# Kernel optimization log

Hardware: AMD Instinct MI355X
Metric: run time of the kernel (lower is better)

Reference implementation:

```python
import jax, jax.numpy as jnp
import numpy as np

B = 8          # graphs per batch
N_PER = 8192   # nodes per graph (equal-sized graphs -> static topk shapes)
N = B * N_PER  # 65536 total nodes
DEG = 16
E = DEG * N    # 1,048,576 edges
C = 64         # conv_width


def setup_inputs() -> dict:
    key = jax.random.key(0)
    ks = jax.random.split(key, 32)
    epg = E // B
    g = jnp.arange(E, dtype=jnp.int32) // epg            # graph id per edge
    src = jax.random.randint(ks[0], (E,), 0, N_PER, dtype=jnp.int32) + g * N_PER
    dst = jax.random.randint(ks[1], (E,), 0, N_PER, dtype=jnp.int32) + g * N_PER

    def w(k, shape, fan_in):
        return (jax.random.normal(k, shape) / np.sqrt(fan_in)).astype(jnp.float32)

    inp = {
        "x": jax.random.normal(ks[2], (N, 2), dtype=jnp.float32),
        "edge_index": jnp.stack([src, dst]),
        # SAGEConv i: out = mean_agg @ wl + x @ wr + b
        "w1l": w(ks[3], (2, C), 2),  "w1r": w(ks[4], (2, C), 2),  "b1": jnp.zeros((C,), jnp.float32),
        "w2l": w(ks[5], (C, C), C),  "w2r": w(ks[6], (C, C), C),  "b2": jnp.zeros((C,), jnp.float32),
        "w3l": w(ks[7], (C, C), C),  "w3r": w(ks[8], (C, C), C),  "b3": jnp.zeros((C,), jnp.float32),
        # GCNConv
        "w4": w(ks[9], (C, C), C),   "b4": jnp.zeros((C,), jnp.float32),
        # TopKPooling score vectors
        "p1": w(ks[10], (C,), C), "p2": w(ks[11], (C,), C),
        "p3": w(ks[12], (C,), C), "p4": w(ks[13], (C,), C),
        # MLP head
        "lw1": w(ks[14], (2 * C, 128), 2 * C), "lb1": jnp.zeros((128,), jnp.float32),
        "lw2": w(ks[15], (128, 64), 128),      "lb2": jnp.zeros((64,), jnp.float32),
        "lw3": w(ks[16], (64, 1), 64),         "lb3": jnp.zeros((1,), jnp.float32),
    }
    return inp


def _sage(x, src, dst, em, wl, wr, b):
    # PyG SAGEConv: lin_l(mean of in-neighbors) + lin_r(x); masked edges contribute 0
    n = x.shape[0]
    s = jax.ops.segment_sum(x[src] * em[:, None], dst, num_segments=n)
    cnt = jax.ops.segment_sum(em, dst, num_segments=n)
    mean = s / jnp.maximum(cnt, 1.0)[:, None]
    return mean @ wl + x @ wr + b


def _gcn(x, src, dst, em, w, b):
    # PyG GCNConv with added self-loops, symmetric normalization
    n = x.shape[0]
    xw = x @ w
    deg = jax.ops.segment_sum(em, dst, num_segments=n) + 1.0  # +1 self-loop
    dinv = jax.lax.rsqrt(deg)
    coef = (dinv[src] * dinv[dst] * em)[:, None]
    agg = jax.ops.segment_sum(xw[src] * coef, dst, num_segments=n)
    return agg + xw / deg[:, None] + b  # self-loop term: deg^-0.5 * deg^-0.5


def _pool(x, src, dst, em, p, nb):
    # TopKPooling(ratio=0.5): score = x.p/||p||, keep top half per graph, scale by tanh
    n = x.shape[0]
    npg = n // nb
    k = npg // 2
    score = x @ p / jnp.linalg.norm(p)
    _, idx = jax.lax.top_k(score.reshape(nb, npg), k)          # [nb, k] local idx
    perm = (idx + (jnp.arange(nb, dtype=idx.dtype) * npg)[:, None]).reshape(-1)
    xn = x[perm] * jnp.tanh(score[perm])[:, None]
    o2n = jnp.full((n,), -1, jnp.int32).at[perm].set(jnp.arange(nb * k, dtype=jnp.int32))
    ns, nd = o2n[src], o2n[dst]
    nm = em * ((ns >= 0) & (nd >= 0)).astype(em.dtype)         # filter_adj via mask
    return xn, jnp.maximum(ns, 0), jnp.maximum(nd, 0), nm


def _readout(x, nb):
    # cat([global_max_pool, global_mean_pool])
    npg = x.shape[0] // nb
    batch = jnp.repeat(jnp.arange(nb), npg)
    mx = jax.ops.segment_max(x, batch, num_segments=nb)
    mn = jax.ops.segment_sum(x, batch, num_segments=nb) / npg
    return jnp.concatenate([mx, mn], axis=1)


def reference(x, edge_index, w1l, w1r, b1, w2l, w2r, b2, w3l, w3r, b3, w4, b4,
              p1, p2, p3, p4, lw1, lb1, lw2, lb2, lw3, lb3):
    src, dst = edge_index[0], edge_index[1]
    em = jnp.ones((src.shape[0],), jnp.float32)

    h = jax.nn.relu(_sage(x, src, dst, em, w1l, w1r, b1))
    h, src, dst, em = _pool(h, src, dst, em, p1, B)
    x1 = _readout(h, B)

    h = jax.nn.relu(_sage(h, src, dst, em, w2l, w2r, b2))
    h, src, dst, em = _pool(h, src, dst, em, p2, B)
    x2 = _readout(h, B)

    h = jax.nn.relu(_sage(h, src, dst, em, w3l, w3r, b3))
    h, src, dst, em = _pool(h, src, dst, em, p3, B)
    x3 = _readout(h, B)  # computed but unused, matching original (x = x1 + x2)

    h = jax.nn.relu(_gcn(h, src, dst, em, w4, b4))
    h, src, dst, em = _pool(h, src, dst, em, p4, B)
    x4 = _readout(h, B)  # computed but unused, matching original

    z = x1 + x2
    z = jax.nn.relu(z @ lw1 + lb1)
    z = jax.nn.relu(z @ lw2 + lb2)
    return z @ lw3 + lb3  # [B, 1]
```

## Files before the change

### kernel.cpp

```cpp
#include <hip/hip_runtime.h>
#include <stdint.h>
#include <math.h>

#define NB 8
#define NPG0 8192
#define EPG 131072
#define P1 16
#define MAXDEG 64

__global__ __launch_bounds__(1024)
void k_aggp(const int* __restrict__ src, const int* __restrict__ dst,
            const float* __restrict__ x, float* __restrict__ partial)
{
    __shared__ float acc[3 * 2048];
    int b = blockIdx.x;
    int g = b >> 6, qq = (b >> 4) & 3, sl = b & 15;
    int tid = threadIdx.x;
    float4* acc4 = (float4*)acc;
    float4 z4 = make_float4(0.f, 0.f, 0.f, 0.f);
    acc4[tid] = z4;
    if (tid < 512) acc4[1024 + tid] = z4;
    __syncthreads();
    int e0 = g * EPG + sl * (EPG / P1);
    int nbase = g * NPG0 + qq * 2048;
    #pragma unroll
    for (int k = 0; k < EPG / P1 / 1024; ++k) {
        int e = e0 + k * 1024 + tid;
        int d = dst[e];
        unsigned local = (unsigned)(d - nbase);
        if (local < 2048u) {
            int s = src[e];
            float2 xv = reinterpret_cast<const float2*>(x)[s];
            atomicAdd(&acc[local], xv.x);
            atomicAdd(&acc[2048 + local], xv.y);
            atomicAdd(&acc[4096 + local], 1.0f);
        }
    }
    __syncthreads();
    float4* o = (float4*)(partial + (size_t)b * 6144);
    o[tid] = acc4[tid];
    if (tid < 512) o[1024 + tid] = acc4[1024 + tid];
}

__global__ void k_aggr(const float* __restrict__ partial, float* __restrict__ agg,
                       int n0)
{
    int t = blockIdx.x * 256 + threadIdx.x;
    if (t >= 3 * n0) return;
    int c = t / n0, node = t - c * n0;
    int g = node >> 13, local = node & (NPG0 - 1);
    int qq = local >> 11, ll = local & 2047;
    const float* p = partial + (size_t)(g * 64 + qq * 16) * 6144 + c * 2048 + ll;
    float s = 0.0f;
    #pragma unroll
    for (int q = 0; q < P1; ++q) s += p[(size_t)q * 6144];
    agg[t] = s;
}

__global__ void k_sage1(const float* __restrict__ x, const float* __restrict__ agg,
                        const float* __restrict__ w1l, const float* __restrict__ w1r,
                        const float* __restrict__ b1, const float* __restrict__ p1,
                        float* __restrict__ h1, float* __restrict__ s1, int n)
{
    int tid  = threadIdx.x;
    int lane = tid & 63;
    int i    = blockIdx.x * 4 + (tid >> 6);
    if (i >= n) return;
    float c   = agg[2 * n + i];
    float inv = 1.0f / fmaxf(c, 1.0f);
    float m0 = agg[i] * inv, m1 = agg[n + i] * inv;
    float2 xv = reinterpret_cast<const float2*>(x)[i];
    float h = m0 * w1l[lane] + m1 * w1l[64 + lane]
            + xv.x * w1r[lane] + xv.y * w1r[64 + lane] + b1[lane];
    h = fmaxf(h, 0.0f);
    h1[i * 64 + lane] = h;
    float pv = p1[lane];
    float num = h * pv, nrm = pv * pv;
    #pragma unroll
    for (int o = 32; o; o >>= 1) {
        num += __shfl_xor(num, o);
        nrm += __shfl_xor(nrm, o);
    }
    if (lane == 0) s1[i] = num / sqrtf(nrm);
}

__device__ __forceinline__ unsigned scan1024(unsigned val, volatile unsigned* ws)
{
    int tid = threadIdx.x, lane = tid & 63, wid = tid >> 6;
    unsigned sc = val;
    #pragma unroll
    for (int off = 1; off < 64; off <<= 1) {
        unsigned t = __shfl_up(sc, off);
        if (lane >= off) sc += t;
    }
    if (lane == 63) ws[wid] = sc;
    __syncthreads();
    if (tid < 16) {
        unsigned w = ws[tid];
        #pragma unroll
        for (int off = 1; off < 16; off <<= 1) {
            unsigned t = __shfl_up(w, off);
            if (tid >= off) w += t;
        }
        ws[tid] = w;
    }
    __syncthreads();
    return sc + (wid ? ws[wid - 1] : 0u);
}

template <int NPG>
__global__ __launch_bounds__(1024)
void k_pool_sel(const float* __restrict__ score, int* __restrict__ n2o,
                int* __restrict__ o2n, int K)
{
    __shared__ unsigned key[NPG];
    __shared__ unsigned hist[1024];
    __shared__ unsigned ws[16];
    __shared__ unsigned long long cand[1024];
    __shared__ int sT1, sR1, sT2, sR2, selCnt, c3;
    int g = blockIdx.x, tid = threadIdx.x;
    if (tid == 0) { selCnt = 0; c3 = 0; }
    hist[tid] = 0u;
    if (o2n) for (int i = tid; i < NPG; i += 1024) o2n[g * NPG + i] = -1;
    __syncthreads();
    for (int i = tid; i < NPG; i += 1024) {
        unsigned b = __float_as_uint(score[g * NPG + i]);
        unsigned u = (b & 0x80000000u) ? ~b : (b | 0x80000000u);
        key[i] = u;
        atomicAdd(&hist[u >> 22], 1u);
    }
    __syncthreads();
    {
        unsigned S = scan1024(hist[1023 - tid], ws);
        int b = 1023 - tid;
        unsigned h = hist[b];
        if (S >= (unsigned)K && S - h < (unsigned)K) { sT1 = b; sR1 = K - (int)(S - h); }
    }
    __syncthreads();
    int T1 = sT1, R1 = sR1;
    for (int i = tid; i < NPG; i += 1024) {
        if ((int)(key[i] >> 22) > T1) {
            int s = atomicAdd(&selCnt, 1);
            int oldid = g * NPG + i;
            n2o[g * K + s] = oldid;
            if (o2n) o2n[oldid] = g * K + s;
        }
    }
    __syncthreads();
    hist[tid] = 0u;
    __syncthreads();
    for (int i = tid; i < NPG; i += 1024)
        if ((int)(key[i] >> 22) == T1) atomicAdd(&hist[(key[i] >> 12) & 1023u], 1u);
    __syncthreads();
    {
        unsigned S = scan1024(hist[1023 - tid], ws);
        int b = 1023 - tid;
        unsigned h = hist[b];
        if (S >= (unsigned)R1 && S - h < (unsigned)R1) { sT2 = b; sR2 = R1 - (int)(S - h); }
    }
    __syncthreads();
    int T2 = sT2, R2 = sR2;
    for (int i = tid; i < NPG; i += 1024) {
        unsigned u = key[i];
        if ((int)(u >> 22) == T1) {
            int b2 = (int)((u >> 12) & 1023u);
            if (b2 > T2) {
                int s = atomicAdd(&selCnt, 1);
                int oldid = g * NPG + i;
                n2o[g * K + s] = oldid;
                if (o2n) o2n[oldid] = g * K + s;
            } else if (b2 == T2) {
                int c = atomicAdd(&c3, 1);
                if (c < 1024)
                    cand[c] = ((unsigned long long)u << 32) | (unsigned)(NPG - 1 - i);
            }
        }
    }
    __syncthreads();
    int M = min(c3, 1024);
    for (int t = tid; t < M; t += 1024) {
        unsigned long long k0 = cand[t];
        int rank = 0;
        for (int j = 0; j < M; ++j) rank += (cand[j] > k0);
        if (rank < R2) {
            int i = NPG - 1 - (int)(k0 & 0xFFFFFFFFu);
            int s = atomicAdd(&selCnt, 1);
            int oldid = g * NPG + i;
            n2o[g * K + s] = oldid;
            if (o2n) o2n[oldid] = g * K + s;
        }
    }
}

__global__ void k_gather(const float* __restrict__ h, const int* __restrict__ n2o,
                         const float* __restrict__ sc, float* __restrict__ hp, int n)
{
    int idx = blockIdx.x * 256 + threadIdx.x;
    int j = idx >> 4, cg = idx & 15;
    if (j >= n) return;
    int oldid = n2o[j];
    float t = tanhf(sc[oldid]);
    float4 v = reinterpret_cast<const float4*>(h)[oldid * 16 + cg];
    v.x *= t; v.y *= t; v.z *= t; v.w *= t;
    reinterpret_cast<float4*>(hp)[idx] = v;
}

__global__ __launch_bounds__(1024)
void k_readout_p(const float* __restrict__ h, const int* __restrict__ n2o,
                 const float* __restrict__ sc, int npg,
                 float* __restrict__ pmx, float* __restrict__ psm)
{
    int g = blockIdx.x >> 4, sl = blockIdx.x & 15;
    int tid = threadIdx.x;
    int cg = tid & 15, rsl = tid >> 4;
    int rpb = npg >> 4;
    float4 mx = make_float4(-INFINITY, -INFINITY, -INFINITY, -INFINITY);
    float4 sm = make_float4(0.f, 0.f, 0.f, 0.f);
    for (int r = rsl; r < rpb; r += 64) {
        int row = g * npg + sl * rpb + r;
        int oldid = n2o ? n2o[row] : row;
        float4 v = reinterpret_cast<const float4*>(h)[oldid * 16 + cg];
        if (sc) {
            float t = tanhf(sc[oldid]);
            v.x *= t; v.y *= t; v.z *= t; v.w *= t;
        }
        mx.x = fmaxf(mx.x, v.x); mx.y = fmaxf(mx.y, v.y);
        mx.z = fmaxf(mx.z, v.z); mx.w = fmaxf(mx.w, v.w);
        sm.x += v.x; sm.y += v.y; sm.z += v.z; sm.w += v.w;
    }
    __shared__ float4 smx[1024], ssm[1024];
    smx[tid] = mx; ssm[tid] = sm;
    __syncthreads();
    for (int s = 32; s >= 1; s >>= 1) {
        if (rsl < s) {
            float4 a = smx[tid], b = smx[tid + s * 16];
            a.x = fmaxf(a.x, b.x); a.y = fmaxf(a.y, b.y);
            a.z = fmaxf(a.z, b.z); a.w = fmaxf(a.w, b.w);
            smx[tid] = a;
            float4 c = ssm[tid], d = ssm[tid + s * 16];
            c.x += d.x; c.y += d.y; c.z += d.z; c.w += d.w;
            ssm[tid] = c;
        }
        __syncthreads();
    }
    if (rsl == 0) {
        reinterpret_cast<float4*>(pmx)[(g * 16 + sl) * 16 + cg] = smx[tid];
        reinterpret_cast<float4*>(psm)[(g * 16 + sl) * 16 + cg] = ssm[tid];
    }
}

__global__ void k_build(const int* __restrict__ src, const int* __restrict__ dst,
                        const int* __restrict__ o2n, int* __restrict__ cnt,
                        int* __restrict__ slots, int E)
{
    int e = blockIdx.x * 256 + threadIdx.x;
    if (e >= E) return;
    int ns = o2n[src[e]], nd = o2n[dst[e]];
    if (ns >= 0 && nd >= 0) {
        int pos = atomicAdd(&cnt[nd], 1);
        if (pos < MAXDEG) slots[nd * MAXDEG + pos] = ns;
    }
}

__global__ __launch_bounds__(256)
void k_sage2(const float* __restrict__ hp, const int* __restrict__ cnt,
             const int* __restrict__ slots,
             const float* __restrict__ w2l, const float* __restrict__ w2r,
             const float* __restrict__ b2, const float* __restrict__ p2,
             float* __restrict__ h2, float* __restrict__ s2)
{
    __shared__ float Xs[64 * 128];
    __shared__ float Wt[64 * 128];
    int tid = threadIdx.x, blk = blockIdx.x;

    #pragma unroll
    for (int i = 0; i < 32; ++i) {
        int idx = i * 256 + tid;
        int k = idx >> 6, c = idx & 63;
        float w = (k < 64) ? w2l[k * 64 + c] : w2r[(k - 64) * 64 + c];
        int slot = (k >> 2) ^ ((c >> 2) & 7);
        Wt[c * 128 + slot * 4 + (k & 3)] = w;
    }

    {
        int n = tid >> 2, p = tid & 3;
        int j = blk * 64 + n;
        int dg = cnt[j];
        int lim = min(dg, MAXDEG);
        const int* sl = slots + j * MAXDEG;
        const float4* hp4 = reinterpret_cast<const float4*>(hp);
        float4 a[4];
        #pragma unroll
        for (int u = 0; u < 4; ++u) a[u] = make_float4(0.f, 0.f, 0.f, 0.f);
        int e = 0;
        for (; e + 1 < lim; e += 2) {
            int r0 = sl[e] * 16 + p * 4;
            int r1 = sl[e + 1] * 16 + p * 4;
            float4 v[4], u4[4];
            #pragma unroll
            for (int u = 0; u < 4; ++u) v[u] = hp4[r0 + u];
            #pragma unroll
            for (int u = 0; u < 4; ++u) u4[u] = hp4[r1 + u];
            #pragma unroll
            for (int u = 0; u < 4; ++u) {
                a[u].x += v[u].x + u4[u].x; a[u].y += v[u].y + u4[u].y;
                a[u].z += v[u].z + u4[u].z; a[u].w += v[u].w + u4[u].w;
            }
        }
        if (e < lim) {
            int r0 = sl[e] * 16 + p * 4;
            #pragma unroll
            for (int u = 0; u < 4; ++u) {
                float4 v = hp4[r0 + u];
                a[u].x += v.x; a[u].y += v.y; a[u].z += v.z; a[u].w += v.w;
            }
        }
        float inv = 1.0f / fmaxf((float)dg, 1.0f);
        int swz = (n >> 2) & 7;
        float4* X4 = reinterpret_cast<float4*>(Xs);
        #pragma unroll
        for (int u = 0; u < 4; ++u) {
            float4 m = a[u];
            m.x *= inv; m.y *= inv; m.z *= inv; m.w *= inv;
            X4[n * 32 + ((p * 4 + u) ^ swz)] = m;
        }
        #pragma unroll
        for (int u = 0; u < 4; ++u)
            X4[n * 32 + ((16 + p * 4 + u) ^ swz)] = hp4[j * 16 + p * 4 + u];
    }
    __syncthreads();

    int rt = tid >> 4, ct = tid & 15;
    int r0 = rt * 4, c0 = ct * 4;
    int swa = rt & 7, swb = ct & 7;
    const float4* Xf = reinterpret_cast<const float4*>(Xs);
    const float4* Wf = reinterpret_cast<const float4*>(Wt);
    float acc[4][4];
    #pragma unroll
    for (int i = 0; i < 4; ++i)
        #pragma unroll
        for (int jq = 0; jq < 4; ++jq) acc[i][jq] = 0.f;
    #pragma unroll 8
    for (int ks = 0; ks < 32; ++ks) {
        float4 aa[4], bb[4];
        #pragma unroll
        for (int i = 0; i < 4; ++i) aa[i] = Xf[(r0 + i) * 32 + (ks ^ swa)];
        #pragma unroll
        for (int jq = 0; jq < 4; ++jq) bb[jq] = Wf[(c0 + jq) * 32 + (ks ^ swb)];
        #pragma unroll
        for (int i = 0; i < 4; ++i)
            #pragma unroll
            for (int jq = 0; jq < 4; ++jq)
                acc[i][jq] += aa[i].x * bb[jq].x + aa[i].y * bb[jq].y
                            + aa[i].z * bb[jq].z + aa[i].w * bb[jq].w;
    }

    float4 b2v = reinterpret_cast<const float4*>(b2)[ct];
    float4 p2v = reinterpret_cast<const float4*>(p2)[ct];
    float nrm = p2v.x * p2v.x + p2v.y * p2v.y + p2v.z * p2v.z + p2v.w * p2v.w;
    float sp[4];
    float4* h2f = reinterpret_cast<float4*>(h2);
    #pragma unroll
    for (int i = 0; i < 4; ++i) {
        float4 o;
        o.x = fmaxf(acc[i][0] + b2v.x, 0.f);
        o.y = fmaxf(acc[i][1] + b2v.y, 0.f);
        o.z = fmaxf(acc[i][2] + b2v.z, 0.f);
        o.w = fmaxf(acc[i][3] + b2v.w, 0.f);
        h2f[(blk * 64 + r0 + i) * 16 + ct] = o;
        sp[i] = o.x * p2v.x + o.y * p2v.y + o.z * p2v.z + o.w * p2v.w;
    }
    #pragma unroll
    for (int o = 1; o < 16; o <<= 1) {
        #pragma unroll
        for (int i = 0; i < 4; ++i) sp[i] += __shfl_xor(sp[i], o);
        nrm += __shfl_xor(nrm, o);
    }
    if (ct == 0) {
        float r = rsqrtf(nrm);
        #pragma unroll
        for (int i = 0; i < 4; ++i) s2[blk * 64 + r0 + i] = sp[i] * r;
    }
}

__global__ __launch_bounds__(128)
void k_mlp(const float* __restrict__ pmx1, const float* __restrict__ psm1,
           const float* __restrict__ pmx2, const float* __restrict__ psm2,
           int npg1, int npg2,
           const float* __restrict__ lw1, const float* __restrict__ lb1,
           const float* __restrict__ lw2, const float* __restrict__ lb2,
           const float* __restrict__ lw3, const float* __restrict__ lb3,
           float* __restrict__ out)
{
    __shared__ float z[NB][128], o1[NB][128], o2[NB][64];
    int tid = threadIdx.x;
    for (int g = 0; g < NB; ++g) {
        float v;
        if (tid < 64) {
            float m1 = -INFINITY, m2 = -INFINITY;
            #pragma unroll
            for (int sl = 0; sl < 16; ++sl) {
                m1 = fmaxf(m1, pmx1[(g * 16 + sl) * 64 + tid]);
                m2 = fmaxf(m2, pmx2[(g * 16 + sl) * 64 + tid]);
            }
            v = m1 + m2;
        } else {
            int ch = tid - 64;
            float s1 = 0.f, s2 = 0.f;
            #pragma unroll
            for (int sl = 0; sl < 16; ++sl) {
                s1 += psm1[(g * 16 + sl) * 64 + ch];
                s2 += psm2[(g * 16 + sl) * 64 + ch];
            }
            v = s1 / (float)npg1 + s2 / (float)npg2;
        }
        z[g][tid] = v;
    }
    __syncthreads();
    for (int g = 0; g < NB; ++g) {
        float a = lb1[tid];
        for (int i = 0; i < 128; ++i) a += z[g][i] * lw1[i * 128 + tid];
        o1[g][tid] = fmaxf(a, 0.0f);
    }
    __syncthreads();
    if (tid < 64) {
        for (int g = 0; g < NB; ++g) {
            float a = lb2[tid];
            for (int i = 0; i < 128; ++i) a += o1[g][i] * lw2[i * 64 + tid];
            o2[g][tid] = fmaxf(a, 0.0f);
        }
    }
    __syncthreads();
    if (tid < NB) {
        int g = tid;
        float a = lb3[0];
        for (int i = 0; i < 64; ++i) a += o2[g][i] * lw3[i];
        out[g] = a;
    }
}

extern "C" void kernel_launch(void* const* d_in, const int* in_sizes, int n_in,
                              void* d_out, int out_size, void* d_ws, size_t ws_size,
                              hipStream_t stream)
{
    (void)n_in; (void)out_size; (void)ws_size;
    const float* x   = (const float*)d_in[0];
    const int*   ei  = (const int*)d_in[1];
    const float* w1l = (const float*)d_in[2];
    const float* w1r = (const float*)d_in[3];
    const float* b1  = (const float*)d_in[4];
    const float* w2l = (const float*)d_in[5];
    const float* w2r = (const float*)d_in[6];
    const float* b2  = (const float*)d_in[7];
    const float* p1  = (const float*)d_in[13];
    const float* p2  = (const float*)d_in[14];
    const float* lw1 = (const float*)d_in[17];
    const float* lb1 = (const float*)d_in[18];
    const float* lw2 = (const float*)d_in[19];
    const float* lb2 = (const float*)d_in[20];
    const float* lw3 = (const float*)d_in[21];
    const float* lb3 = (const float*)d_in[22];

    const int N0   = in_sizes[0] / 2;
    const int E    = in_sizes[1] / 2;
    const int K1   = NPG0 / 2;
    const int N1   = NB * K1;
    const int K2   = K1 / 2;

    const int* src = ei;
    const int* dst = ei + E;

    char* w = (char*)d_ws;
    auto alloc = [&](size_t bytes) -> char* {
        char* p = w;
        w += (bytes + 255) & ~(size_t)255;
        return p;
    };
    float* partial = (float*)alloc((size_t)NB * 4 * P1 * 6144 * 4);
    float* agg   = (float*)alloc((size_t)3 * N0 * 4);
    int*   cnt2  = (int*)alloc((size_t)N1 * 4);
    int*   slots = (int*)alloc((size_t)N1 * MAXDEG * 4);
    float* h1    = (float*)alloc((size_t)N0 * 64 * 4);
    float* s1    = (float*)alloc((size_t)N0 * 4);
    int*   o2n1  = (int*)alloc((size_t)N0 * 4);
    int*   n2o1  = (int*)alloc((size_t)N1 * 4);
    float* h1p   = (float*)alloc((size_t)N1 * 64 * 4);
    float* h2    = (float*)alloc((size_t)N1 * 64 * 4);
    float* s2    = (float*)alloc((size_t)N1 * 4);
    int*   n2o2  = (int*)alloc((size_t)(NB * K2) * 4);
    float* pmx1  = (float*)alloc((size_t)NB * 16 * 64 * 4);
    float* psm1  = (float*)alloc((size_t)NB * 16 * 64 * 4);
    float* pmx2  = (float*)alloc((size_t)NB * 16 * 64 * 4);
    float* psm2  = (float*)alloc((size_t)NB * 16 * 64 * 4);

    hipMemsetAsync(cnt2, 0, (size_t)N1 * 4, stream);

    k_aggp<<<NB * 4 * P1, 1024, 0, stream>>>(src, dst, x, partial);
    k_aggr<<<(3 * N0 + 255) / 256, 256, 0, stream>>>(partial, agg, N0);
    k_sage1<<<N0 / 4, 256, 0, stream>>>(x, agg, w1l, w1r, b1, p1, h1, s1, N0);
    k_pool_sel<8192><<<NB, 1024, 0, stream>>>(s1, n2o1, o2n1, K1);
    k_gather<<<N1 * 16 / 256, 256, 0, stream>>>(h1, n2o1, s1, h1p, N1);
    k_readout_p<<<NB * 16, 1024, 0, stream>>>(h1p, nullptr, nullptr, K1, pmx1, psm1);
    k_build<<<E / 256, 256, 0, stream>>>(src, dst, o2n1, cnt2, slots, E);
    k_sage2<<<N1 / 64, 256, 0, stream>>>(h1p, cnt2, slots, w2l, w2r, b2, p2, h2, s2);
    k_pool_sel<4096><<<NB, 1024, 0, stream>>>(s2, n2o2, nullptr, K2);
    k_readout_p<<<NB * 16, 1024, 0, stream>>>(h2, n2o2, s2, K2, pmx2, psm2);
    k_mlp<<<1, 128, 0, stream>>>(pmx1, psm1, pmx2, psm2, K1, K2,
                                 lw1, lb1, lw2, lb2, lw3, lb3, (float*)d_out);
}
```

Measured before the change: 144.8 us.

## Fuse partial reduction into SAGE1 scoring and recompute h1 in pooled readout

Merges the partial-sum reduction with the first SAGE layer's score computation so the full h1 tensor is never written. Only per-node mean features (float2) are stored, and the pooled h1p is recomputed from them inside a fused gather+readout kernel. This removes roughly 16MB of h1 traffic and two kernel launches. The edge loops in aggregation and adjacency build are also vectorized to int4 loads, which adds some per-thread serial work and recomputes the 64-wide dot product twice.

```diff
diff --git a/kernel.cpp b/kernel.cpp
--- a/kernel.cpp
+++ b/kernel.cpp
@@ -23,17 +23,24 @@
     __syncthreads();
     int e0 = g * EPG + sl * (EPG / P1);
     int nbase = g * NPG0 + qq * 2048;
-    #pragma unroll
-    for (int k = 0; k < EPG / P1 / 1024; ++k) {
-        int e = e0 + k * 1024 + tid;
-        int d = dst[e];
-        unsigned local = (unsigned)(d - nbase);
-        if (local < 2048u) {
-            int s = src[e];
-            float2 xv = reinterpret_cast<const float2*>(x)[s];
-            atomicAdd(&acc[local], xv.x);
-            atomicAdd(&acc[2048 + local], xv.y);
-            atomicAdd(&acc[4096 + local], 1.0f);
+    const float2* x2 = reinterpret_cast<const float2*>(x);
+    #pragma unroll
+    for (int k = 0; k < 2; ++k) {
+        int e = e0 + (k * 1024 + tid) * 4;
+        int4 d4 = *reinterpret_cast<const int4*>(dst + e);
+        unsigned l0 = (unsigned)(d4.x - nbase), l1 = (unsigned)(d4.y - nbase);
+        unsigned l2 = (unsigned)(d4.z - nbase), l3 = (unsigned)(d4.w - nbase);
+        bool v0 = l0 < 2048u, v1 = l1 < 2048u, v2 = l2 < 2048u, v3 = l3 < 2048u;
+        if (v0 | v1 | v2 | v3) {
+            int4 s4 = *reinterpret_cast<const int4*>(src + e);
+            if (v0) { float2 xv = x2[s4.x]; atomicAdd(&acc[l0], xv.x);
+                      atomicAdd(&acc[2048 + l0], xv.y); atomicAdd(&acc[4096 + l0], 1.0f); }
+            if (v1) { float2 xv = x2[s4.y]; atomicAdd(&acc[l1], xv.x);
+                      atomicAdd(&acc[2048 + l1], xv.y); atomicAdd(&acc[4096 + l1], 1.0f); }
+            if (v2) { float2 xv = x2[s4.z]; atomicAdd(&acc[l2], xv.x);
+                      atomicAdd(&acc[2048 + l2], xv.y); atomicAdd(&acc[4096 + l2], 1.0f); }
+            if (v3) { float2 xv = x2[s4.w]; atomicAdd(&acc[l3], xv.x);
+                      atomicAdd(&acc[2048 + l3], xv.y); atomicAdd(&acc[4096 + l3], 1.0f); }
         }
     }
     __syncthreads();
@@ -42,46 +49,36 @@
     if (tid < 512) o[1024 + tid] = acc4[1024 + tid];
 }
 
-__global__ void k_aggr(const float* __restrict__ partial, float* __restrict__ agg,
-                       int n0)
-{
-    int t = blockIdx.x * 256 + threadIdx.x;
-    if (t >= 3 * n0) return;
-    int c = t / n0, node = t - c * n0;
+__global__ __launch_bounds__(256)
+void k_sage1f(const float* __restrict__ partial, const float* __restrict__ x,
+              const float* __restrict__ w1l, const float* __restrict__ w1r,
+              const float* __restrict__ b1, const float* __restrict__ p1,
+              float2* __restrict__ mv, float* __restrict__ s1)
+{
+    int tid = threadIdx.x;
+    int node = blockIdx.x * 256 + tid;
     int g = node >> 13, local = node & (NPG0 - 1);
     int qq = local >> 11, ll = local & 2047;
-    const float* p = partial + (size_t)(g * 64 + qq * 16) * 6144 + c * 2048 + ll;
-    float s = 0.0f;
-    #pragma unroll
-    for (int q = 0; q < P1; ++q) s += p[(size_t)q * 6144];
-    agg[t] = s;
-}
-
-__global__ void k_sage1(const float* __restrict__ x, const float* __restrict__ agg,
-                        const float* __restrict__ w1l, const float* __restrict__ w1r,
-                        const float* __restrict__ b1, const float* __restrict__ p1,
-                        float* __restrict__ h1, float* __restrict__ s1, int n)
-{
-    int tid  = threadIdx.x;
-    int lane = tid & 63;
-    int i    = blockIdx.x * 4 + (tid >> 6);
-    if (i >= n) return;
-    float c   = agg[2 * n + i];
-    float inv = 1.0f / fmaxf(c, 1.0f);
-    float m0 = agg[i] * inv, m1 = agg[n + i] * inv;
-    float2 xv = reinterpret_cast<const float2*>(x)[i];
-    float h = m0 * w1l[lane] + m1 * w1l[64 + lane]
-            + xv.x * w1r[lane] + xv.y * w1r[64 + lane] + b1[lane];
-    h = fmaxf(h, 0.0f);
-    h1[i * 64 + lane] = h;
-    float pv = p1[lane];
-    float num = h * pv, nrm = pv * pv;
-    #pragma unroll
-    for (int o = 32; o; o >>= 1) {
-        num += __shfl_xor(num, o);
-        nrm += __shfl_xor(nrm, o);
-    }
-    if (lane == 0) s1[i] = num / sqrtf(nrm);
+    const float* p = partial + (size_t)(g * 64 + qq * 16) * 6144 + ll;
+    float s0 = 0.f, s1v = 0.f, sc = 0.f;
+    #pragma unroll
+    for (int q = 0; q < 16; ++q) {
+        const float* pq = p + (size_t)q * 6144;
+        s0 += pq[0]; s1v += pq[2048]; sc += pq[4096];
+    }
+    float inv = 1.0f / fmaxf(sc, 1.0f);
+    float m0 = s0 * inv, m1 = s1v * inv;
+    float2 xv = reinterpret_cast<const float2*>(x)[node];
+    mv[node] = make_float2(m0, m1);
+    float num = 0.f, nrm = 0.f;
+    #pragma unroll 8
+    for (int c = 0; c < 64; ++c) {
+        float h = fmaxf(m0 * w1l[c] + m1 * w1l[64 + c]
+                      + xv.x * w1r[c] + xv.y * w1r[64 + c] + b1[c], 0.0f);
+        float pv = p1[c];
+        num += h * pv; nrm += pv * pv;
+    }
+    s1[node] = num / sqrtf(nrm);
 }
 
 __device__ __forceinline__ unsigned scan1024(unsigned val, volatile unsigned* ws)
@@ -192,17 +189,61 @@
     }
 }
 
-__global__ void k_gather(const float* __restrict__ h, const int* __restrict__ n2o,
-                         const float* __restrict__ sc, float* __restrict__ hp, int n)
-{
-    int idx = blockIdx.x * 256 + threadIdx.x;
-    int j = idx >> 4, cg = idx & 15;
-    if (j >= n) return;
-    int oldid = n2o[j];
-    float t = tanhf(sc[oldid]);
-    float4 v = reinterpret_cast<const float4*>(h)[oldid * 16 + cg];
-    v.x *= t; v.y *= t; v.z *= t; v.w *= t;
-    reinterpret_cast<float4*>(hp)[idx] = v;
+__global__ __launch_bounds__(1024)
+void k_ro1(const float2* __restrict__ mv, const float* __restrict__ x,
+           const float* __restrict__ s1, const int* __restrict__ n2o,
+           const float* __restrict__ w1l, const float* __restrict__ w1r,
+           const float* __restrict__ b1, int npg, float* __restrict__ hp,
+           float* __restrict__ pmx, float* __restrict__ psm)
+{
+    int g = blockIdx.x >> 4, sl = blockIdx.x & 15;
+    int tid = threadIdx.x;
+    int cg = tid & 15, rsl = tid >> 4;
+    int rpb = npg >> 4;
+    int c0 = cg * 4;
+    float4 wl0 = *reinterpret_cast<const float4*>(w1l + c0);
+    float4 wl1 = *reinterpret_cast<const float4*>(w1l + 64 + c0);
+    float4 wr0 = *reinterpret_cast<const float4*>(w1r + c0);
+    float4 wr1 = *reinterpret_cast<const float4*>(w1r + 64 + c0);
+    float4 bb  = *reinterpret_cast<const float4*>(b1 + c0);
+    const float2* x2 = reinterpret_cast<const float2*>(x);
+    float4 mx = make_float4(-INFINITY, -INFINITY, -INFINITY, -INFINITY);
+    float4 sm = make_float4(0.f, 0.f, 0.f, 0.f);
+    for (int r = rsl; r < rpb; r += 64) {
+        int row = g * npg + sl * rpb + r;
+        int old = n2o[row];
+        float2 m = mv[old];
+        float2 xv = x2[old];
+        float t = tanhf(s1[old]);
+        float4 v;
+        v.x = fmaxf(m.x * wl0.x + m.y * wl1.x + xv.x * wr0.x + xv.y * wr1.x + bb.x, 0.f) * t;
+        v.y = fmaxf(m.x * wl0.y + m.y * wl1.y + xv.x * wr0.y + xv.y * wr1.y + bb.y, 0.f) * t;
+        v.z = fmaxf(m.x * wl0.z + m.y * wl1.z + xv.x * wr0.z + xv.y * wr1.z + bb.z, 0.f) * t;
+        v.w = fmaxf(m.x * wl0.w + m.y * wl1.w + xv.x * wr0.w + xv.y * wr1.w + bb.w, 0.f) * t;
+        reinterpret_cast<float4*>(hp)[row * 16 + cg] = v;
+        mx.x = fmaxf(mx.x, v.x); mx.y = fmaxf(mx.y, v.y);
+        mx.z = fmaxf(mx.z, v.z); mx.w = fmaxf(mx.w, v.w);
+        sm.x += v.x; sm.y += v.y; sm.z += v.z; sm.w += v.w;
+    }
+    __shared__ float4 smx[1024], ssm[1024];
+    smx[tid] = mx; ssm[tid] = sm;
+    __syncthreads();
+    for (int s = 32; s >= 1; s >>= 1) {
+        if (rsl < s) {
+            float4 a = smx[tid], b = smx[tid + s * 16];
+            a.x = fmaxf(a.x, b.x); a.y = fmaxf(a.y, b.y);
+            a.z = fmaxf(a.z, b.z); a.w = fmaxf(a.w, b.w);
+            smx[tid] = a;
+            float4 c = ssm[tid], d = ssm[tid + s * 16];
+            c.x += d.x; c.y += d.y; c.z += d.z; c.w += d.w;
+            ssm[tid] = c;
+        }
+        __syncthreads();
+    }
+    if (rsl == 0) {
+        reinterpret_cast<float4*>(pmx)[(g * 16 + sl) * 16 + cg] = smx[tid];
+        reinterpret_cast<float4*>(psm)[(g * 16 + sl) * 16 + cg] = ssm[tid];
+    }
 }
 
 __global__ __launch_bounds__(1024)
@@ -253,12 +294,19 @@
                         const int* __restrict__ o2n, int* __restrict__ cnt,
                         int* __restrict__ slots, int E)
 {
-    int e = blockIdx.x * 256 + threadIdx.x;
+    int e = (blockIdx.x * 256 + threadIdx.x) * 4;
     if (e >= E) return;
-    int ns = o2n[src[e]], nd = o2n[dst[e]];
-    if (ns >= 0 && nd >= 0) {
-        int pos = atomicAdd(&cnt[nd], 1);
-        if (pos < MAXDEG) slots[nd * MAXDEG + pos] = ns;
+    int4 s4 = *reinterpret_cast<const int4*>(src + e);
+    int4 d4 = *reinterpret_cast<const int4*>(dst + e);
+    #pragma unroll
+    for (int i = 0; i < 4; ++i) {
+        int sv = (i == 0) ? s4.x : (i == 1) ? s4.y : (i == 2) ? s4.z : s4.w;
+        int dv = (i == 0) ? d4.x : (i == 1) ? d4.y : (i == 2) ? d4.z : d4.w;
+        int ns = o2n[sv], nd = o2n[dv];
+        if (ns >= 0 && nd >= 0) {
+            int pos = atomicAdd(&cnt[nd], 1);
+            if (pos < MAXDEG) slots[nd * MAXDEG + pos] = ns;
+        }
     }
 }
 
@@ -476,32 +524,30 @@
         w += (bytes + 255) & ~(size_t)255;
         return p;
     };
-    float* partial = (float*)alloc((size_t)NB * 4 * P1 * 6144 * 4);
-    float* agg   = (float*)alloc((size_t)3 * N0 * 4);
-    int*   cnt2  = (int*)alloc((size_t)N1 * 4);
-    int*   slots = (int*)alloc((size_t)N1 * MAXDEG * 4);
-    float* h1    = (float*)alloc((size_t)N0 * 64 * 4);
-    float* s1    = (float*)alloc((size_t)N0 * 4);
-    int*   o2n1  = (int*)alloc((size_t)N0 * 4);
-    int*   n2o1  = (int*)alloc((size_t)N1 * 4);
-    float* h1p   = (float*)alloc((size_t)N1 * 64 * 4);
-    float* h2    = (float*)alloc((size_t)N1 * 64 * 4);
-    float* s2    = (float*)alloc((size_t)N1 * 4);
-    int*   n2o2  = (int*)alloc((size_t)(NB * K2) * 4);
-    float* pmx1  = (float*)alloc((size_t)NB * 16 * 64 * 4);
-    float* psm1  = (float*)alloc((size_t)NB * 16 * 64 * 4);
-    float* pmx2  = (float*)alloc((size_t)NB * 16 * 64 * 4);
-    float* psm2  = (float*)alloc((size_t)NB * 16 * 64 * 4);
+    float*  partial = (float*)alloc((size_t)NB * 4 * P1 * 6144 * 4);
+    float2* mv    = (float2*)alloc((size_t)N0 * 8);
+    int*    cnt2  = (int*)alloc((size_t)N1 * 4);
+    int*    slots = (int*)alloc((size_t)N1 * MAXDEG * 4);
+    float*  s1    = (float*)alloc((size_t)N0 * 4);
+    int*    o2n1  = (int*)alloc((size_t)N0 * 4);
+    int*    n2o1  = (int*)alloc((size_t)N1 * 4);
+    float*  h1p   = (float*)alloc((size_t)N1 * 64 * 4);
+    float*  h2    = (float*)alloc((size_t)N1 * 64 * 4);
+    float*  s2    = (float*)alloc((size_t)N1 * 4);
+    int*    n2o2  = (int*)alloc((size_t)(NB * K2) * 4);
+    float*  pmx1  = (float*)alloc((size_t)NB * 16 * 64 * 4);
+    float*  psm1  = (float*)alloc((size_t)NB * 16 * 64 * 4);
+    float*  pmx2  = (float*)alloc((size_t)NB * 16 * 64 * 4);
+    float*  psm2  = (float*)alloc((size_t)NB * 16 * 64 * 4);
 
     hipMemsetAsync(cnt2, 0, (size_t)N1 * 4, stream);
 
     k_aggp<<<NB * 4 * P1, 1024, 0, stream>>>(src, dst, x, partial);
-    k_aggr<<<(3 * N0 + 255) / 256, 256, 0, stream>>>(partial, agg, N0);
-    k_sage1<<<N0 / 4, 256, 0, stream>>>(x, agg, w1l, w1r, b1, p1, h1, s1, N0);
+    k_sage1f<<<N0 / 256, 256, 0, stream>>>(partial, x, w1l, w1r, b1, p1, mv, s1);
     k_pool_sel<8192><<<NB, 1024, 0, stream>>>(s1, n2o1, o2n1, K1);
-    k_gather<<<N1 * 16 / 256, 256, 0, stream>>>(h1, n2o1, s1, h1p, N1);
-    k_readout_p<<<NB * 16, 1024, 0, stream>>>(h1p, nullptr, nullptr, K1, pmx1, psm1);
-    k_build<<<E / 256, 256, 0, stream>>>(src, dst, o2n1, cnt2, slots, E);
+    k_ro1<<<NB * 16, 1024, 0, stream>>>(mv, x, s1, n2o1, w1l, w1r, b1, K1,
+                                        h1p, pmx1, psm1);
+    k_build<<<E / 1024, 256, 0, stream>>>(src, dst, o2n1, cnt2, slots, E);
     k_sage2<<<N1 / 64, 256, 0, stream>>>(h1p, cnt2, slots, w2l, w2r, b2, p2, h2, s2);
     k_pool_sel<4096><<<NB, 1024, 0, stream>>>(s2, n2o2, nullptr, K2);
     k_readout_p<<<NB * 16, 1024, 0, stream>>>(h2, n2o2, s2, K2, pmx2, psm2);
```

Measured after the change: 135.0 us. -6.7%, faster.
